# Kernel optimization log

Measured on AMD Instinct MI355X. Metric: run time of the kernel, lower is better.

## Reference

```python
import jax, jax.numpy as jnp
import numpy as np

HEADS = 8

def setup_inputs() -> dict:
    key = jax.random.key(0)
    ks = jax.random.split(key, 10)
    B, C, D, W, H = 4, 256, 12, 12, 12
    dk = C // HEADS
    return {
        "x": jax.random.normal(ks[0], (B, C, D, W, H), jnp.float32),
        "wq": jax.random.normal(ks[1], (C, C), jnp.float32) * 0.05,
        "bq": jax.random.normal(ks[2], (C,), jnp.float32) * 0.05,
        "wk": jax.random.normal(ks[3], (C, C), jnp.float32) * 0.05,
        "bk": jax.random.normal(ks[4], (C,), jnp.float32) * 0.05,
        "wv": jax.random.normal(ks[5], (C, C), jnp.float32) * 0.05,
        "bv": jax.random.normal(ks[6], (C,), jnp.float32) * 0.05,
        "rel_d": jax.random.normal(ks[7], (1, HEADS, dk, D, 1, 1), jnp.float32),
        "rel_h": jax.random.normal(ks[8], (1, HEADS, dk, 1, 1, H), jnp.float32),
        "rel_w": jax.random.normal(ks[9], (1, HEADS, dk, 1, W, 1), jnp.float32),
    }


def reference(x, wq, bq, wk, bk, wv, bv, rel_d, rel_h, rel_w):
    B, C, D, W, H = x.shape
    dk = C // HEADS
    N = D * W * H

    def proj(w, b):
        # Conv3d kernel_size=1 == per-voxel linear over channels
        y = jnp.einsum('bcdwh,oc->bodwh', x, w) + b[None, :, None, None, None]
        return y.reshape(B, HEADS, dk, N)  # [B,h,dk,N]

    q = proj(wq, bq)
    k = proj(wk, bk)
    v = proj(wv, bv)

    # content-content: q^T k -> [B,h,N,N]
    cc = jnp.einsum('bhdn,bhdm->bhnm', q, k)
    # relative-position bias: (rel_h+rel_w+rel_d) broadcasts to [1,h,dk,D,W,H]
    pos = (rel_h + rel_w + rel_d).reshape(1, HEADS, dk, N)
    # content-position: pos^T @ q -> [B,h,N,N]
    cp = jnp.einsum('bhdn,bhdm->bhnm', pos, q)

    attn = jax.nn.softmax(cc + cp, axis=-1)  # [B,h,N,N]
    # out = v @ attn^T -> [B,h,dk,N]
    out = jnp.einsum('bhdn,bhmn->bhdm', v, attn)
    return out.reshape(B, C, D, W, H)
```

## Files before the change

kernel.cpp:

```cpp
#include <hip/hip_runtime.h>
#include <math.h>

#define HEADS 8
#define DK 32
#define B_ 4
#define C_ 256
#define NVOX 1728
#define DE 64
#define PITCH 72
#define XPITCH 136
#define CPITCH 36
#define LOG2E 1.44269504088896f

typedef _Float16 f16x8 __attribute__((ext_vector_type(8)));
typedef __fp16 fp16x2 __attribute__((ext_vector_type(2)));
typedef float f32x16 __attribute__((ext_vector_type(16)));

__device__ inline float h2f(short s) {
    _Float16 h = *(_Float16*)&s;
    return (float)h;
}
__device__ inline f32x16 mfma32h(f16x8 a, f16x8 b, f32x16 c) {
    return __builtin_amdgcn_mfma_f32_32x32x16_f16(a, b, c, 0, 0, 0);
}

union H8 { _Float16 h[8]; uint4 v; };
union H4 { _Float16 h[4]; uint2 v; };

__global__ __launch_bounds__(256)
void prep_kernel(const float* __restrict__ x,
                 const float* __restrict__ wq, const float* __restrict__ wk,
                 const float* __restrict__ wv,
                 const float* __restrict__ rel_d, const float* __restrict__ rel_h,
                 const float* __restrict__ rel_w,
                 short* __restrict__ wf, short* __restrict__ xf,
                 short* __restrict__ Qf) {
    __shared__ float tile[64][65];
    int bid = blockIdx.x;
    int t = threadIdx.x;

    if (bid < 192) {
        int idx = (bid * 256 + t) * 4;
        int m = idx >> 16;
        const float* w = (m == 0) ? wq : (m == 1) ? wk : wv;
        float4 v = *(const float4*)&w[idx & 65535];
        H4 hh;
        hh.h[0] = (_Float16)v.x; hh.h[1] = (_Float16)v.y;
        hh.h[2] = (_Float16)v.z; hh.h[3] = (_Float16)v.w;
        *(uint2*)&wf[idx] = hh.v;
    } else if (bid < 624) {
        int q = bid - 192;
        int nb = (q % 27) * 64;
        int c0 = ((q / 27) % 4) * 64;
        int b  = q / 108;
        const float* xb = x + (size_t)b * C_ * NVOX;
        for (int e = t; e < 4096; e += 256) {
            int ci = e >> 6, nl = e & 63;
            tile[ci][nl] = xb[(size_t)(c0 + ci) * NVOX + nb + nl];
        }
        __syncthreads();
        for (int e = t; e < 512; e += 256) {
            int n = e >> 3, cg = (e & 7) * 8;
            H8 hi;
            #pragma unroll
            for (int j = 0; j < 8; j++) hi.h[j] = (_Float16)tile[cg + j][n];
            *(uint4*)&xf[((size_t)b * NVOX + nb + n) * C_ + c0 + cg] = hi.v;
        }
    } else {
        int q = bid - 624;
        int nb = (q % 27) * 64;
        int h  = (q / 27) % 8;
        int b  = q / 216;
        int bh = b * HEADS + h;
        int nl = t & 63, dd0 = (t >> 6) * 8;
        int n = nb + nl;
        int di = n / 144, wi = (n / 12) % 12, hi = n % 12;
        H8 ph;
        #pragma unroll
        for (int o = 0; o < 8; o++) {
            int hd = h * DK + dd0 + o;
            ph.h[o] = (_Float16)(rel_d[hd * 12 + di] + rel_w[hd * 12 + wi] +
                                 rel_h[hd * 12 + hi]);
        }
        *(uint4*)&Qf[((size_t)bh * NVOX + n) * DE + DK + dd0] = ph.v;
    }
}

struct FS {
    union {
        short xs[64 * XPITCH];
        float cbuf[3][64][CPITCH];
    } u;
};

__global__ __launch_bounds__(384, 4)
void fproj_kernel(const short* __restrict__ xf, const short* __restrict__ wf,
                  const float* __restrict__ bq, const float* __restrict__ bk,
                  const float* __restrict__ bv,
                  short* __restrict__ Qf, short* __restrict__ Kf,
                  short* __restrict__ Vf) {
    __shared__ FS sm;
    int nb = blockIdx.x * 64, h = blockIdx.y, b = blockIdx.z;
    int bh = b * HEADS + h;
    int t = threadIdx.x;
    int w = t >> 6, l = t & 63, ln = l & 31, hv = l >> 5;
    int mat = w >> 1, nh = w & 1;

    const short* xb = xf + ((size_t)b * NVOX + nb) * C_;
    const short* wA = wf + ((size_t)mat * C_ + h * DK + ln) * C_;
    int xrow = (nh * 32 + ln) * XPITCH;

    f32x16 acc;
    #pragma unroll
    for (int r = 0; r < 16; r++) acc[r] = 0.f;

    #pragma unroll 1
    for (int ch = 0; ch < 2; ch++) {
        __syncthreads();
        for (int e = t; e < 1024; e += 384) {
            int row = e >> 4, c8 = (e & 15) * 8;
            *(uint4*)&sm.u.xs[row * XPITCH + c8] =
                *(const uint4*)&xb[row * C_ + ch * 128 + c8];
        }
        __syncthreads();
        #pragma unroll 4
        for (int ks = 0; ks < 8; ks++) {
            int kl_ = ks * 16 + hv * 8;
            f16x8 a = *(const f16x8*)&wA[ch * 128 + kl_];
            f16x8 bfr = *(const f16x8*)&sm.u.xs[xrow + kl_];
            acc = mfma32h(a, bfr, acc);
        }
    }
    __syncthreads();

    const float* bias = (mat == 0) ? bq : (mat == 1) ? bk : bv;
    int ncol = nh * 32 + ln;
    #pragma unroll
    for (int q2 = 0; q2 < 4; q2++) {
        float4 cv;
        float* cvp = (float*)&cv;
        #pragma unroll
        for (int m = 0; m < 4; m++) {
            int o_loc = 8 * q2 + 4 * hv + m;
            cvp[m] = acc[4 * q2 + m] + bias[h * DK + o_loc];
        }
        *(float4*)&sm.u.cbuf[mat][ncol][8 * q2 + 4 * hv] = cv;
    }
    __syncthreads();

    if (t < 256) {
        int n = t >> 2, ddg = (t & 3) * 8;
        H8 qh, kh;
        #pragma unroll
        for (int j = 0; j < 8; j++) {
            qh.h[j] = (_Float16)sm.u.cbuf[0][n][ddg + j];
            kh.h[j] = (_Float16)sm.u.cbuf[1][n][ddg + j];
        }
        *(uint4*)&Qf[((size_t)bh * NVOX + nb + n) * DE + ddg] = qh.v;
        *(uint4*)&Kf[((size_t)bh * NVOX + nb + n) * DK + ddg] = kh.v;
    }
    if (t < 256) {
        int d = t >> 3, ng = (t & 7) * 8;
        H8 vv;
        #pragma unroll
        for (int j = 0; j < 8; j++)
            vv.h[j] = (_Float16)sm.u.cbuf[2][ng + j][d];
        *(uint4*)&Vf[((size_t)bh * DK + d) * NVOX + nb + ng] = vv.v;
    }
}

struct SMem {
    short K[64][PITCH];
    short V[DK][PITCH];
    short P[64][PITCH];
};

__global__ __launch_bounds__(128, 3)
void attn_kernel(const short* __restrict__ Qf, const short* __restrict__ Kf,
                 const short* __restrict__ Vf,
                 short* __restrict__ wsO, float* __restrict__ wsM,
                 float* __restrict__ wsL) {
    __shared__ SMem sm;
    int bx = blockIdx.x;
    int it = bx >> 1, jp = bx & 1;
    int h = blockIdx.y, b = blockIdx.z;
    int bh = b * HEADS + h;
    int t = threadIdx.x;
    int w  = t >> 6;
    int l  = t & 63;
    int ln = l & 31;
    int hv = l >> 5;
    int i_loc  = w * 32 + ln;
    int i_glob = it * 64 + i_loc;

    const short* Qp = Qf + (size_t)bh * NVOX * DE;
    const short* Kp = Kf + (size_t)bh * NVOX * DK;
    const short* Vp = Vf + (size_t)bh * DK * NVOX;

    f16x8 qf[4];
    #pragma unroll
    for (int ks = 0; ks < 4; ks++)
        qf[ks] = *(const f16x8*)&Qp[(size_t)i_glob * DE + ks * 16 + hv * 8];

    float mL = -INFINITY;
    float lsum = 0.f;
    f32x16 O;
    #pragma unroll
    for (int r = 0; r < 16; r++) O[r] = 0.f;

    int jt0 = jp ? 14 : 0, jt1 = jp ? 27 : 14;
    #pragma unroll 1
    for (int jt = jt0; jt < jt1; jt++) {
        int jb = jt * 64;
        __syncthreads();
        for (int e = t; e < 512; e += 128) {
            int row = e >> 3, cq = e & 7, c8 = cq * 8;
            uint4 v = (cq < 4)
                ? *(const uint4*)&Kp[(size_t)(jb + row) * DK + c8]
                : *(const uint4*)&Qp[(size_t)(jb + row) * DE + (c8 - 32)];
            *(uint4*)&sm.K[row][c8] = v;
        }
        for (int e = t; e < 256; e += 128) {
            int d = e >> 3, c = (e & 7) * 8;
            *(uint4*)&sm.V[d][c] = *(const uint4*)&Vp[(size_t)d * NVOX + jb + c];
        }
        __syncthreads();

        f32x16 sc[2];
        #pragma unroll
        for (int js = 0; js < 2; js++) {
            f32x16 s;
            #pragma unroll
            for (int r = 0; r < 16; r++) s[r] = 0.f;
            #pragma unroll
            for (int ks = 0; ks < 4; ks++) {
                f16x8 kfr = *(const f16x8*)&sm.K[js * 32 + ln][ks * 16 + hv * 8];
                s = mfma32h(kfr, qf[ks], s);
            }
            sc[js] = s;
        }

        float mx = sc[0][0];
        #pragma unroll
        for (int js = 0; js < 2; js++)
            #pragma unroll
            for (int r = 0; r < 16; r++) mx = fmaxf(mx, sc[js][r]);
        mx = fmaxf(mx, __shfl_xor(mx, 32));
        float mLn = fmaxf(mL, mx * LOG2E);
        float alpha = exp2f(mL - mLn);
        mL = mLn;
        float ps = 0.f;
        #pragma unroll
        for (int js = 0; js < 2; js++)
            #pragma unroll
            for (int r = 0; r < 16; r++) {
                float p = exp2f(fmaf(sc[js][r], LOG2E, -mLn));
                sc[js][r] = p;
                ps += p;
            }
        ps += __shfl_xor(ps, 32);
        lsum = lsum * alpha + ps;

        #pragma unroll
        for (int js = 0; js < 2; js++)
            #pragma unroll
            for (int g = 0; g < 4; g++) {
                union { fp16x2 h2[2]; uint2 v; } pk;
                pk.h2[0] = __builtin_amdgcn_cvt_pkrtz(sc[js][4 * g + 0], sc[js][4 * g + 1]);
                pk.h2[1] = __builtin_amdgcn_cvt_pkrtz(sc[js][4 * g + 2], sc[js][4 * g + 3]);
                *(uint2*)&sm.P[i_loc][js * 32 + g * 8 + hv * 4] = pk.v;
            }

        #pragma unroll
        for (int r = 0; r < 16; r++) O[r] *= alpha;
        #pragma unroll
        for (int ks = 0; ks < 4; ks++) {
            f16x8 va = *(const f16x8*)&sm.V[ln][ks * 16 + hv * 8];
            f16x8 pb = *(const f16x8*)&sm.P[i_loc][ks * 16 + hv * 8];
            O = mfma32h(va, pb, O);
        }
    }

    short* Op = wsO + ((size_t)jp * (B_ * HEADS) + bh) * DK * NVOX;
    #pragma unroll
    for (int r = 0; r < 16; r++) {
        int d = (r & 3) + 8 * (r >> 2) + 4 * hv;
        _Float16 oh = (_Float16)O[r];
        Op[(size_t)d * NVOX + i_glob] = *(short*)&oh;
    }
    if (hv == 0) {
        size_t mo = ((size_t)jp * (B_ * HEADS) + bh) * NVOX + i_glob;
        wsM[mo] = mL;
        wsL[mo] = lsum;
    }
}

__global__ void combine_kernel(const short* __restrict__ wsO,
                               const float* __restrict__ wsM,
                               const float* __restrict__ wsL,
                               float* __restrict__ out) {
    int idx = (blockIdx.x * 256 + threadIdx.x) * 4;
    int i = idx % NVOX;
    int bh = (idx / NVOX) >> 5;
    const size_t oh = (size_t)B_ * HEADS * DK * NVOX;
    const size_t mh = (size_t)B_ * HEADS * NVOX;
    size_t mo = (size_t)bh * NVOX + i;
    float4 m0 = *(const float4*)&wsM[mo];
    float4 m1 = *(const float4*)&wsM[mh + mo];
    float4 l0 = *(const float4*)&wsL[mo];
    float4 l1 = *(const float4*)&wsL[mh + mo];
    uint2 o0u = *(const uint2*)&wsO[idx];
    uint2 o1u = *(const uint2*)&wsO[oh + idx];
    const short* o0s = (const short*)&o0u;
    const short* o1s = (const short*)&o1u;
    const float* m0p = (const float*)&m0; const float* m1p = (const float*)&m1;
    const float* l0p = (const float*)&l0; const float* l1p = (const float*)&l1;
    float4 res;
    float* rp = (float*)&res;
    #pragma unroll
    for (int j = 0; j < 4; j++) {
        float m = fmaxf(m0p[j], m1p[j]);
        float a0 = exp2f(m0p[j] - m), a1 = exp2f(m1p[j] - m);
        rp[j] = (a0 * h2f(o0s[j]) + a1 * h2f(o1s[j])) /
                (a0 * l0p[j] + a1 * l1p[j]);
    }
    *(float4*)&out[idx] = res;
}

extern "C" void kernel_launch(void* const* d_in, const int* in_sizes, int n_in,
                              void* d_out, int out_size, void* d_ws, size_t ws_size,
                              hipStream_t stream) {
    const float* x     = (const float*)d_in[0];
    const float* wq    = (const float*)d_in[1];
    const float* bq    = (const float*)d_in[2];
    const float* wk    = (const float*)d_in[3];
    const float* bk    = (const float*)d_in[4];
    const float* wv    = (const float*)d_in[5];
    const float* bv    = (const float*)d_in[6];
    const float* rel_d = (const float*)d_in[7];
    const float* rel_h = (const float*)d_in[8];
    const float* rel_w = (const float*)d_in[9];
    float* out = (float*)d_out;

    size_t qksz = (size_t)B_ * HEADS * NVOX * DE;
    size_t vsz  = (size_t)B_ * HEADS * DK * NVOX;
    short* Qf  = (short*)d_ws;
    short* Kf  = Qf + qksz;
    short* Vf  = Kf + vsz;
    short* wf  = Vf + vsz;
    short* wsO = wf + (size_t)3 * C_ * C_;
    float* wsM = (float*)(wsO + 2 * vsz);
    float* wsL = wsM + 2 * (size_t)B_ * HEADS * NVOX;
    short* xf  = wsO;

    prep_kernel<<<dim3(1488), dim3(256), 0, stream>>>(
        x, wq, wk, wv, rel_d, rel_h, rel_w, wf, xf, Qf);
    fproj_kernel<<<dim3(NVOX / 64, HEADS, B_), dim3(384), 0, stream>>>(
        xf, wf, bq, bk, bv, Qf, Kf, Vf);
    attn_kernel<<<dim3(2 * NVOX / 64, HEADS, B_), dim3(128), 0, stream>>>(
        Qf, Kf, Vf, wsO, wsM, wsL);
    combine_kernel<<<dim3((int)(vsz / 1024)), dim3(256), 0, stream>>>(wsO, wsM, wsL, out);
}
```

Before: 158.2 us.

## Double-buffer attention tiles via direct global-to-LDS loads and split keys three ways

```diff
diff --git a/kernel.cpp b/kernel.cpp
--- a/kernel.cpp
+++ b/kernel.cpp
@@ -7,10 +7,11 @@
 #define C_ 256
 #define NVOX 1728
 #define DE 64
-#define PITCH 72
 #define XPITCH 136
 #define CPITCH 36
 #define LOG2E 1.44269504088896f
+#define JSPLIT 3
+#define NJT 9
 
 typedef _Float16 f16x8 __attribute__((ext_vector_type(8)));
 typedef __fp16 fp16x2 __attribute__((ext_vector_type(2)));
@@ -23,9 +24,15 @@
 __device__ inline f32x16 mfma32h(f16x8 a, f16x8 b, f32x16 c) {
     return __builtin_amdgcn_mfma_f32_32x32x16_f16(a, b, c, 0, 0, 0);
 }
+__device__ __forceinline__ void gl_lds16(const short* g, short* l) {
+    __builtin_amdgcn_global_load_lds(
+        (const __attribute__((address_space(1))) unsigned int*)g,
+        (__attribute__((address_space(3))) unsigned int*)l, 16, 0, 0);
+}
 
 union H8 { _Float16 h[8]; uint4 v; };
 union H4 { _Float16 h[4]; uint2 v; };
+union PW { fp16x2 h2; unsigned int u; };
 
 __global__ __launch_bounds__(256)
 void prep_kernel(const float* __restrict__ x,
@@ -169,20 +176,15 @@
     }
 }
 
-struct SMem {
-    short K[64][PITCH];
-    short V[DK][PITCH];
-    short P[64][PITCH];
-};
-
 __global__ __launch_bounds__(128, 3)
 void attn_kernel(const short* __restrict__ Qf, const short* __restrict__ Kf,
                  const short* __restrict__ Vf,
                  short* __restrict__ wsO, float* __restrict__ wsM,
                  float* __restrict__ wsL) {
-    __shared__ SMem sm;
+    __shared__ __align__(16) short Ksm[2][4096];
+    __shared__ __align__(16) short Vsm[2][2048];
     int bx = blockIdx.x;
-    int it = bx >> 1, jp = bx & 1;
+    int it = bx / JSPLIT, jp = bx % JSPLIT;
     int h = blockIdx.y, b = blockIdx.z;
     int bh = b * HEADS + h;
     int t = threadIdx.x;
@@ -202,29 +204,46 @@
     for (int ks = 0; ks < 4; ks++)
         qf[ks] = *(const f16x8*)&Qp[(size_t)i_glob * DE + ks * 16 + hv * 8];
 
+    int jb0 = jp * NJT * 64;
+
+    const short* gk0 = Kp + (size_t)(jb0 + (l ^ (w + 0))) * DK + (w + 0) * 8;
+    const short* gk1 = Kp + (size_t)(jb0 + (l ^ (w + 2))) * DK + (w + 2) * 8;
+    const short* gk2 = Qp + (size_t)(jb0 + (l ^ (w + 4))) * DE + (w + 0) * 8;
+    const short* gk3 = Qp + (size_t)(jb0 + (l ^ (w + 6))) * DE + (w + 2) * 8;
+    int vb0 = 2 * w + hv, vb1 = 2 * w + 4 + hv;
+    const short* gv0 = Vp + (size_t)(ln ^ vb0) * NVOX + jb0 + vb0 * 8;
+    const short* gv1 = Vp + (size_t)(ln ^ vb1) * NVOX + jb0 + vb1 * 8;
+
+#define STAGE(bufp) do {                                   \
+        short* kl_ = &Ksm[bufp][0];                        \
+        short* vl_ = &Vsm[bufp][0];                        \
+        gl_lds16(gk0, kl_ + (w + 0) * 512);                \
+        gl_lds16(gk1, kl_ + (w + 2) * 512);                \
+        gl_lds16(gk2, kl_ + (w + 4) * 512);                \
+        gl_lds16(gk3, kl_ + (w + 6) * 512);                \
+        gl_lds16(gv0, vl_ + (w + 0) * 512);                \
+        gl_lds16(gv1, vl_ + (w + 2) * 512);                \
+        gk0 += 64 * DK; gk1 += 64 * DK;                    \
+        gk2 += 64 * DE; gk3 += 64 * DE;                    \
+        gv0 += 64; gv1 += 64;                              \
+    } while (0)
+
     float mL = -INFINITY;
     float lsum = 0.f;
     f32x16 O;
     #pragma unroll
     for (int r = 0; r < 16; r++) O[r] = 0.f;
 
-    int jt0 = jp ? 14 : 0, jt1 = jp ? 27 : 14;
+    STAGE(0);
+
     #pragma unroll 1
-    for (int jt = jt0; jt < jt1; jt++) {
-        int jb = jt * 64;
+    for (int jt = 0; jt < NJT; ++jt) {
+        int buf = jt & 1;
         __syncthreads();
-        for (int e = t; e < 512; e += 128) {
-            int row = e >> 3, cq = e & 7, c8 = cq * 8;
-            uint4 v = (cq < 4)
-                ? *(const uint4*)&Kp[(size_t)(jb + row) * DK + c8]
-                : *(const uint4*)&Qp[(size_t)(jb + row) * DE + (c8 - 32)];
-            *(uint4*)&sm.K[row][c8] = v;
-        }
-        for (int e = t; e < 256; e += 128) {
-            int d = e >> 3, c = (e & 7) * 8;
-            *(uint4*)&sm.V[d][c] = *(const uint4*)&Vp[(size_t)d * NVOX + jb + c];
-        }
-        __syncthreads();
+        if (jt + 1 < NJT) STAGE(buf ^ 1);
+
+        const short* Kb = &Ksm[buf][0];
+        const short* Vb = &Vsm[buf][0];
 
         f32x16 sc[2];
         #pragma unroll
@@ -234,52 +253,73 @@
             for (int r = 0; r < 16; r++) s[r] = 0.f;
             #pragma unroll
             for (int ks = 0; ks < 4; ks++) {
-                f16x8 kfr = *(const f16x8*)&sm.K[js * 32 + ln][ks * 16 + hv * 8];
+                int kb = ks * 2 + hv;
+                f16x8 kfr = *(const f16x8*)&Kb[kb * 512 + js * 256 + (ln ^ kb) * 8];
                 s = mfma32h(kfr, qf[ks], s);
             }
             sc[js] = s;
         }
 
-        float mx = sc[0][0];
-        #pragma unroll
-        for (int js = 0; js < 2; js++)
+        float m0 = fmaxf(sc[0][0], sc[1][0]);
+        float m1 = fmaxf(sc[0][1], sc[1][1]);
+        float m2 = fmaxf(sc[0][2], sc[1][2]);
+        float m3 = fmaxf(sc[0][3], sc[1][3]);
+        #pragma unroll
+        for (int r = 4; r < 16; r += 4) {
+            m0 = fmaxf(m0, fmaxf(sc[0][r + 0], sc[1][r + 0]));
+            m1 = fmaxf(m1, fmaxf(sc[0][r + 1], sc[1][r + 1]));
+            m2 = fmaxf(m2, fmaxf(sc[0][r + 2], sc[1][r + 2]));
+            m3 = fmaxf(m3, fmaxf(sc[0][r + 3], sc[1][r + 3]));
+        }
+        float mx = fmaxf(fmaxf(m0, m1), fmaxf(m2, m3));
+        mx = fmaxf(mx, __shfl_xor(mx, 32));
+        float mxl = mx * LOG2E;
+        if (!__all(mxl <= mL + 4.0f)) {
+            float mLn = fmaxf(mL, mxl);
+            float alpha = exp2f(mL - mLn);
+            mL = mLn;
+            lsum *= alpha;
             #pragma unroll
-            for (int r = 0; r < 16; r++) mx = fmaxf(mx, sc[js][r]);
-        mx = fmaxf(mx, __shfl_xor(mx, 32));
-        float mLn = fmaxf(mL, mx * LOG2E);
-        float alpha = exp2f(mL - mLn);
-        mL = mLn;
-        float ps = 0.f;
-        #pragma unroll
-        for (int js = 0; js < 2; js++)
+            for (int r = 0; r < 16; r++) O[r] *= alpha;
+        }
+
+        float ps0 = 0.f, ps1 = 0.f, ps2 = 0.f, ps3 = 0.f;
+        #pragma unroll
+        for (int js = 0; js < 2; js++) {
             #pragma unroll
-            for (int r = 0; r < 16; r++) {
-                float p = exp2f(fmaf(sc[js][r], LOG2E, -mLn));
-                sc[js][r] = p;
-                ps += p;
+            for (int r = 0; r < 16; r += 4) {
+                float p0 = exp2f(fmaf(sc[js][r + 0], LOG2E, -mL));
+                float p1 = exp2f(fmaf(sc[js][r + 1], LOG2E, -mL));
+                float p2 = exp2f(fmaf(sc[js][r + 2], LOG2E, -mL));
+                float p3 = exp2f(fmaf(sc[js][r + 3], LOG2E, -mL));
+                sc[js][r + 0] = p0; sc[js][r + 1] = p1;
+                sc[js][r + 2] = p2; sc[js][r + 3] = p3;
+                ps0 += p0; ps1 += p1; ps2 += p2; ps3 += p3;
             }
+        }
+        float ps = (ps0 + ps1) + (ps2 + ps3);
         ps += __shfl_xor(ps, 32);
-        lsum = lsum * alpha + ps;
-
-        #pragma unroll
-        for (int js = 0; js < 2; js++)
-            #pragma unroll
-            for (int g = 0; g < 4; g++) {
-                union { fp16x2 h2[2]; uint2 v; } pk;
-                pk.h2[0] = __builtin_amdgcn_cvt_pkrtz(sc[js][4 * g + 0], sc[js][4 * g + 1]);
-                pk.h2[1] = __builtin_amdgcn_cvt_pkrtz(sc[js][4 * g + 2], sc[js][4 * g + 3]);
-                *(uint2*)&sm.P[i_loc][js * 32 + g * 8 + hv * 4] = pk.v;
-            }
-
-        #pragma unroll
-        for (int r = 0; r < 16; r++) O[r] *= alpha;
+        lsum += ps;
+
         #pragma unroll
         for (int ks = 0; ks < 4; ks++) {
-            f16x8 va = *(const f16x8*)&sm.V[ln][ks * 16 + hv * 8];
-            f16x8 pb = *(const f16x8*)&sm.P[i_loc][ks * 16 + hv * 8];
-            O = mfma32h(va, pb, O);
-        }
-    }
+            int js = ks >> 1, u8 = (ks & 1) * 8;
+            PW a0, a1, b0, b1;
+            a0.h2 = __builtin_amdgcn_cvt_pkrtz(sc[js][u8 + 0], sc[js][u8 + 1]);
+            a1.h2 = __builtin_amdgcn_cvt_pkrtz(sc[js][u8 + 2], sc[js][u8 + 3]);
+            b0.h2 = __builtin_amdgcn_cvt_pkrtz(sc[js][u8 + 4], sc[js][u8 + 5]);
+            b1.h2 = __builtin_amdgcn_cvt_pkrtz(sc[js][u8 + 6], sc[js][u8 + 7]);
+            auto r0 = __builtin_amdgcn_permlane32_swap(a0.u, b0.u, false, false);
+            auto r1 = __builtin_amdgcn_permlane32_swap(a1.u, b1.u, false, false);
+            union { unsigned int w4[4]; f16x8 f; } pb;
+            pb.w4[0] = r0[0]; pb.w4[1] = r1[0];
+            pb.w4[2] = r0[1]; pb.w4[3] = r1[1];
+            int vb = ks * 2 + hv;
+            f16x8 va = *(const f16x8*)&Vb[vb * 256 + (ln ^ vb) * 8];
+            O = mfma32h(va, pb.f, O);
+        }
+    }
+#undef STAGE
 
     short* Op = wsO + ((size_t)jp * (B_ * HEADS) + bh) * DK * NVOX;
     #pragma unroll
@@ -307,22 +347,30 @@
     size_t mo = (size_t)bh * NVOX + i;
     float4 m0 = *(const float4*)&wsM[mo];
     float4 m1 = *(const float4*)&wsM[mh + mo];
+    float4 m2 = *(const float4*)&wsM[2 * mh + mo];
     float4 l0 = *(const float4*)&wsL[mo];
     float4 l1 = *(const float4*)&wsL[mh + mo];
+    float4 l2 = *(const float4*)&wsL[2 * mh + mo];
     uint2 o0u = *(const uint2*)&wsO[idx];
     uint2 o1u = *(const uint2*)&wsO[oh + idx];
+    uint2 o2u = *(const uint2*)&wsO[2 * oh + idx];
     const short* o0s = (const short*)&o0u;
     const short* o1s = (const short*)&o1u;
+    const short* o2s = (const short*)&o2u;
     const float* m0p = (const float*)&m0; const float* m1p = (const float*)&m1;
+    const float* m2p = (const float*)&m2;
     const float* l0p = (const float*)&l0; const float* l1p = (const float*)&l1;
+    const float* l2p = (const float*)&l2;
     float4 res;
     float* rp = (float*)&res;
     #pragma unroll
     for (int j = 0; j < 4; j++) {
-        float m = fmaxf(m0p[j], m1p[j]);
-        float a0 = exp2f(m0p[j] - m), a1 = exp2f(m1p[j] - m);
-        rp[j] = (a0 * h2f(o0s[j]) + a1 * h2f(o1s[j])) /
-                (a0 * l0p[j] + a1 * l1p[j]);
+        float m = fmaxf(fmaxf(m0p[j], m1p[j]), m2p[j]);
+        float a0 = exp2f(m0p[j] - m);
+        float a1 = exp2f(m1p[j] - m);
+        float a2 = exp2f(m2p[j] - m);
+        rp[j] = (a0 * h2f(o0s[j]) + a1 * h2f(o1s[j]) + a2 * h2f(o2s[j])) /
+                (a0 * l0p[j] + a1 * l1p[j] + a2 * l2p[j]);
     }
     *(float4*)&out[idx] = res;
 }
@@ -349,15 +397,15 @@
     short* Vf  = Kf + vsz;
     short* wf  = Vf + vsz;
     short* wsO = wf + (size_t)3 * C_ * C_;
-    float* wsM = (float*)(wsO + 2 * vsz);
-    float* wsL = wsM + 2 * (size_t)B_ * HEADS * NVOX;
+    float* wsM = (float*)(wsO + 3 * vsz);
+    float* wsL = wsM + 3 * (size_t)B_ * HEADS * NVOX;
     short* xf  = wsO;
 
     prep_kernel<<<dim3(1488), dim3(256), 0, stream>>>(
         x, wq, wk, wv, rel_d, rel_h, rel_w, wf, xf, Qf);
     fproj_kernel<<<dim3(NVOX / 64, HEADS, B_), dim3(384), 0, stream>>>(
         xf, wf, bq, bk, bv, Qf, Kf, Vf);
-    attn_kernel<<<dim3(2 * NVOX / 64, HEADS, B_), dim3(128), 0, stream>>>(
+    attn_kernel<<<dim3(JSPLIT * NVOX / 64, HEADS, B_), dim3(128), 0, stream>>>(
         Qf, Kf, Vf, wsO, wsM, wsL);
     combine_kernel<<<dim3((int)(vsz / 1024)), dim3(256), 0, stream>>>(wsO, wsM, wsL, out);
 }
```

Result: no change. 158.9 us (+0.5%).
